# Kernel tuning notes

Measured on AMD Instinct MI355X. Metric: run time of the kernel, lower is better.

The kernel has to match this reference:

```python
import jax, jax.numpy as jnp
import numpy as np

B, N, M = 8, 2048, 2048
DQ = DK = DV = H = O = 1024

def setup_inputs() -> dict:
    key = jax.random.key(0)
    ks = jax.random.split(key, 10)
    input_query = jax.random.normal(ks[0], (B, N, DQ), dtype=jnp.float32)
    input_key = jax.random.normal(ks[1], (B, M, DK), dtype=jnp.float32)
    input_value = jax.random.normal(ks[2], (B, M, DV), dtype=jnp.float32)
    seq_lens = jax.random.randint(ks[3], (B,), 1, M + 1)
    seq_lens = seq_lens.at[0].set(M)  # original asserts max(seq_lens) == M
    s = 1.0 / np.sqrt(DQ)
    Wq = jax.random.normal(ks[4], (DQ, H), dtype=jnp.float32) * s
    bq = jnp.zeros((H,), dtype=jnp.float32)
    Wk = jax.random.normal(ks[5], (DK, H), dtype=jnp.float32) * s
    bk = jnp.zeros((H,), dtype=jnp.float32)
    Wv = jax.random.normal(ks[6], (DV, O), dtype=jnp.float32) * s
    bv = jnp.zeros((O,), dtype=jnp.float32)
    return {"input_query": input_query, "input_key": input_key, "input_value": input_value,
            "seq_lens": seq_lens, "Wq": Wq, "bq": bq, "Wk": Wk, "bk": bk, "Wv": Wv, "bv": bv}


def reference(input_query, input_key, input_value, seq_lens, Wq, bq, Wk, bk, Wv, bv):
    hidden_dim = Wq.shape[1]
    lq = input_query @ Wq + bq          # (B, N, H)
    lk = input_key @ Wk + bk            # (B, M, H)
    lv = input_value @ Wv + bv          # (B, M, O)
    scores = jnp.einsum('bnh,bmh->bnm', lq, lk) / jnp.sqrt(jnp.float32(hidden_dim))
    # additive mask: 0 for valid positions, finfo.min for padded (as in original)
    valid = (jnp.arange(scores.shape[-1]) < seq_lens[:, None])[:, None, :]  # (B,1,M)
    add_mask = jnp.where(valid, 0.0, jnp.finfo(scores.dtype).min)
    scores = scores + add_mask
    probs = jax.nn.softmax(scores, axis=-1)
    out = jnp.einsum('bnm,bmo->bno', probs, lv)  # dropout is identity in eval
    return out
```

## Files before the change

kernel.cpp:

```cpp
#include <hip/hip_runtime.h>
#include <hip/hip_bf16.h>

typedef unsigned short u16;
typedef __attribute__((ext_vector_type(8))) short bfrag;
typedef __attribute__((ext_vector_type(4))) float f32x4;
typedef __attribute__((ext_vector_type(8))) unsigned short us8;
typedef __attribute__((ext_vector_type(4))) unsigned short us4;

__device__ __forceinline__ u16 f2bf(float f) {
  union { float f; unsigned int u; } x; x.f = f;
  unsigned int r = x.u + 0x7fffu + ((x.u >> 16) & 1u);
  return (u16)(r >> 16);
}
__device__ __forceinline__ float bf2f(u16 u) {
  union { unsigned int u; float f; } x; x.u = ((unsigned int)u) << 16;
  return x.f;
}

__device__ __forceinline__ void gld16(const void* g, void* l) {
  __builtin_amdgcn_global_load_lds((const __attribute__((address_space(1))) void*)g,
                                   (__attribute__((address_space(3))) void*)l, 16, 0, 0);
}

__global__ __launch_bounds__(256) void transpose_w(const float* __restrict__ W0,
                                                   const float* __restrict__ W1,
                                                   const float* __restrict__ W2,
                                                   u16* __restrict__ T0,
                                                   u16* __restrict__ T1,
                                                   u16* __restrict__ T2) {
  const float* W = (blockIdx.z == 0) ? W0 : ((blockIdx.z == 1) ? W1 : W2);
  u16* T = (blockIdx.z == 0) ? T0 : ((blockIdx.z == 1) ? T1 : T2);
  __shared__ u16 tile[64][72];
  const int t = threadIdx.x;
  const int rr = t >> 4;
  const int cc = (t & 15) * 4;
  const int kbase = blockIdx.y * 64, nbase = blockIdx.x * 64;
#pragma unroll
  for (int j = 0; j < 4; ++j) {
    int kl = rr + j * 16;
    float4 v = *(const float4*)(W + (size_t)(kbase + kl) * 1024 + nbase + cc);
    tile[kl][cc + 0] = f2bf(v.x);
    tile[kl][cc + 1] = f2bf(v.y);
    tile[kl][cc + 2] = f2bf(v.z);
    tile[kl][cc + 3] = f2bf(v.w);
  }
  __syncthreads();
#pragma unroll
  for (int j = 0; j < 4; ++j) {
    int nl = rr + j * 16;
    us4 o;
    o[0] = tile[cc + 0][nl];
    o[1] = tile[cc + 1][nl];
    o[2] = tile[cc + 2][nl];
    o[3] = tile[cc + 3][nl];
    *(us4*)(T + (size_t)(nbase + nl) * 1024 + kbase + cc) = o;
  }
}

__global__ __launch_bounds__(256) void cvt_bf16(const float* __restrict__ src,
                                                u16* __restrict__ dst, int n8) {
  int i = blockIdx.x * blockDim.x + threadIdx.x;
  const int stride = gridDim.x * blockDim.x;
  for (; i < n8; i += stride) {
    const float4* p = (const float4*)(src + (size_t)i * 8);
    float4 v0 = p[0], v1 = p[1];
    us8 o;
    o[0] = f2bf(v0.x); o[1] = f2bf(v0.y); o[2] = f2bf(v0.z); o[3] = f2bf(v0.w);
    o[4] = f2bf(v1.x); o[5] = f2bf(v1.y); o[6] = f2bf(v1.z); o[7] = f2bf(v1.w);
    *(us8*)(dst + (size_t)i * 8) = o;
  }
}

template <int OUT>
__global__ __launch_bounds__(512, 2) void gemm256(const u16* __restrict__ gA,
                                                  const u16* __restrict__ gB,
                                                  const float* __restrict__ bias,
                                                  void* __restrict__ outp,
                                                  int K, int ldc) {
  __shared__ u16 lds[65536];
  const int tid = threadIdx.x;

  const int id = blockIdx.x + gridDim.x * blockIdx.y;
  const int bx = (id >> 3) & 3, by = (id & 7) + 8 * (id >> 5);

  const u16* A = gA;
  const u16* B = gB;
  const int brow = by * 256, bcol = bx * 256;

  const int wv = tid >> 6, l = tid & 63;
  const int wm = wv >> 2, wn = wv & 3;
  const int fr = l & 15, fq = l >> 4;
  const int g0 = (fq ^ (fr & 7)) * 8;
  const int g1 = ((4 + fq) ^ (fr & 7)) * 8;

  const int srow = tid >> 3;
  const int sg = (tid & 7) ^ (srow & 7);
  const u16* aS = A + (size_t)(brow + srow) * K + sg * 8;
  const u16* bS = B + (size_t)(bcol + srow) * K + sg * 8;
  u16* const dA = lds + wv * 512;
  u16* const dB = lds + 32768 + wv * 512;

  f32x4 acc[8][4] = {};
  const int NT = K >> 6;

  auto stA = [&](int tile, int c, int buf) {
    gld16(aS + (size_t)tile * 64 + (size_t)c * 64 * K, dA + buf * 16384 + c * 4096);
  };
  auto stB = [&](int tile, int c, int buf) {
    gld16(bS + (size_t)tile * 64 + (size_t)c * 64 * K, dB + buf * 16384 + c * 4096);
  };

#pragma unroll
  for (int c = 0; c < 4; ++c) stA(0, c, 0);
#pragma unroll
  for (int c = 0; c < 4; ++c) stB(0, c, 0);
  if (NT > 1) {
    stA(1, 0, 1); stA(1, 2, 1);
    stB(1, 0, 1); stB(1, 1, 1); stB(1, 2, 1); stB(1, 3, 1);
  }

  for (int t = 0; t < NT; ++t) {
    const int cur = t & 1;
    const u16* At = lds + cur * 16384;
    const u16* Bt = lds + 32768 + cur * 16384;

    if (t + 1 < NT) asm volatile("s_waitcnt vmcnt(6)" ::: "memory");
    else            asm volatile("s_waitcnt vmcnt(0)" ::: "memory");
    __builtin_amdgcn_s_barrier();

    bfrag a[4][2], b[2][2][2];

#pragma unroll
    for (int m = 0; m < 4; ++m) {
      const u16* p = At + (wm * 128 + m * 16 + fr) * 64;
      a[m][0] = *(const bfrag*)(p + g0);
      a[m][1] = *(const bfrag*)(p + g1);
    }
#pragma unroll
    for (int n = 0; n < 2; ++n) {
      const u16* p = Bt + (wn * 64 + n * 16 + fr) * 64;
      b[0][n][0] = *(const bfrag*)(p + g0);
      b[0][n][1] = *(const bfrag*)(p + g1);
    }
    if (t + 1 < NT) { stA(t + 1, 1, cur ^ 1); stA(t + 1, 3, cur ^ 1); }
    __builtin_amdgcn_s_barrier();
    asm volatile("s_waitcnt lgkmcnt(0)" ::: "memory");
    __builtin_amdgcn_sched_barrier(0);
    __builtin_amdgcn_s_setprio(1);
#pragma unroll
    for (int n = 0; n < 2; ++n)
#pragma unroll
      for (int m = 0; m < 4; ++m) {
        acc[m][n] = __builtin_amdgcn_mfma_f32_16x16x32_bf16(a[m][0], b[0][n][0], acc[m][n], 0, 0, 0);
        acc[m][n] = __builtin_amdgcn_mfma_f32_16x16x32_bf16(a[m][1], b[0][n][1], acc[m][n], 0, 0, 0);
      }
    __builtin_amdgcn_s_setprio(0);
    __builtin_amdgcn_s_barrier();

#pragma unroll
    for (int n = 0; n < 2; ++n) {
      const u16* p = Bt + (wn * 64 + 32 + n * 16 + fr) * 64;
      b[1][n][0] = *(const bfrag*)(p + g0);
      b[1][n][1] = *(const bfrag*)(p + g1);
    }
    if (t + 2 < NT) { stA(t + 2, 0, cur); stA(t + 2, 2, cur); }
    __builtin_amdgcn_s_barrier();
    asm volatile("s_waitcnt lgkmcnt(0)" ::: "memory");
    __builtin_amdgcn_sched_barrier(0);
    __builtin_amdgcn_s_setprio(1);
#pragma unroll
    for (int n = 0; n < 2; ++n)
#pragma unroll
      for (int m = 0; m < 4; ++m) {
        acc[m][2 + n] = __builtin_amdgcn_mfma_f32_16x16x32_bf16(a[m][0], b[1][n][0], acc[m][2 + n], 0, 0, 0);
        acc[m][2 + n] = __builtin_amdgcn_mfma_f32_16x16x32_bf16(a[m][1], b[1][n][1], acc[m][2 + n], 0, 0, 0);
      }
    __builtin_amdgcn_s_setprio(0);
    __builtin_amdgcn_s_barrier();

#pragma unroll
    for (int m = 0; m < 4; ++m) {
      const u16* p = At + (wm * 128 + 64 + m * 16 + fr) * 64;
      a[m][0] = *(const bfrag*)(p + g0);
      a[m][1] = *(const bfrag*)(p + g1);
    }
    if (t + 2 < NT) { stB(t + 2, 0, cur); stB(t + 2, 1, cur); }
    __builtin_amdgcn_s_barrier();
    asm volatile("s_waitcnt lgkmcnt(0)" ::: "memory");
    __builtin_amdgcn_sched_barrier(0);
    __builtin_amdgcn_s_setprio(1);
#pragma unroll
    for (int n = 0; n < 2; ++n)
#pragma unroll
      for (int m = 0; m < 4; ++m) {
        acc[4 + m][n] = __builtin_amdgcn_mfma_f32_16x16x32_bf16(a[m][0], b[0][n][0], acc[4 + m][n], 0, 0, 0);
        acc[4 + m][n] = __builtin_amdgcn_mfma_f32_16x16x32_bf16(a[m][1], b[0][n][1], acc[4 + m][n], 0, 0, 0);
      }
    __builtin_amdgcn_s_setprio(0);
    __builtin_amdgcn_s_barrier();

    if (t + 2 < NT) { stB(t + 2, 2, cur); stB(t + 2, 3, cur); }
    __builtin_amdgcn_s_setprio(1);
#pragma unroll
    for (int n = 0; n < 2; ++n)
#pragma unroll
      for (int m = 0; m < 4; ++m) {
        acc[4 + m][2 + n] = __builtin_amdgcn_mfma_f32_16x16x32_bf16(a[m][0], b[1][n][0], acc[4 + m][2 + n], 0, 0, 0);
        acc[4 + m][2 + n] = __builtin_amdgcn_mfma_f32_16x16x32_bf16(a[m][1], b[1][n][1], acc[4 + m][2 + n], 0, 0, 0);
      }
    __builtin_amdgcn_s_setprio(0);
    __builtin_amdgcn_s_barrier();
  }

#pragma unroll
  for (int mg = 0; mg < 8; ++mg) {
    const int r0 = brow + wm * 128 + mg * 16 + fq * 4;
#pragma unroll
    for (int n = 0; n < 4; ++n) {
      const int c = bcol + wn * 64 + n * 16 + fr;
      f32x4 vv = acc[mg][n];
      float bb = bias[c];
      if constexpr (OUT == 0) {
        u16* C = (u16*)outp;
#pragma unroll
        for (int j = 0; j < 4; ++j) C[(size_t)(r0 + j) * ldc + c] = f2bf(vv[j] + bb);
      } else {
        const int bz2 = r0 >> 11, mm = r0 & 2047;
        us4 o;
#pragma unroll
        for (int j = 0; j < 4; ++j) o[j] = f2bf(vv[j] + bb);
        *(us4*)((u16*)outp + ((size_t)bz2 * 1024 + c) * 2048 + mm) = o;
      }
    }
  }
}

template <int OUT>
__global__ __launch_bounds__(512, 4) void gemm128d(const u16* __restrict__ gA,
                                                   const u16* __restrict__ gB,
                                                   void* __restrict__ outp,
                                                   int K, int ldc,
                                                   size_t aStride, size_t bStride,
                                                   size_t cStride,
                                                   const int* __restrict__ seq) {
  __shared__ u16 lds[32768];
  const int tid = threadIdx.x;
  const int bx = blockIdx.x, by = blockIdx.y, bz = blockIdx.z;

  const u16* A = gA + (size_t)bz * aStride;
  const u16* B = gB + (size_t)bz * bStride;
  const int brow = by * 128, bcol = bx * 128;

  int NTe = K >> 6;
  if constexpr (OUT == 1) {
    if (bcol >= seq[bz]) return;
  }
  if constexpr (OUT == 3) {
    const int nt2 = (seq[bz] + 63) >> 6;
    NTe = nt2 < NTe ? nt2 : NTe;
  }

  const int wv = tid >> 6, l = tid & 63;
  const int wm = wv >> 2, wn = wv & 3;
  const int fr = l & 15, fq = l >> 4;
  const int g0 = (fq ^ (fr & 7)) * 8;
  const int g1 = ((4 + fq) ^ (fr & 7)) * 8;

  const int srow = tid >> 3;
  const int sg = (tid & 7) ^ (srow & 7);
  const u16* aS = A + (size_t)(brow + srow) * K + sg * 8;
  const u16* bS = B + (size_t)(bcol + srow) * K + sg * 8;
  u16* const dA = lds + wv * 512;
  u16* const dB = lds + 16384 + wv * 512;

  f32x4 acc[4][2] = {};

  auto stage = [&](int tile, int buf) {
#pragma unroll
    for (int c = 0; c < 2; ++c)
      gld16(aS + (size_t)tile * 64 + (size_t)c * 64 * K, dA + buf * 8192 + c * 4096);
#pragma unroll
    for (int c = 0; c < 2; ++c)
      gld16(bS + (size_t)tile * 64 + (size_t)c * 64 * K, dB + buf * 8192 + c * 4096);
  };

  stage(0, 0);
  asm volatile("s_waitcnt vmcnt(0)" ::: "memory");
  __builtin_amdgcn_s_barrier();

  for (int t = 0; t < NTe; ++t) {
    const int cur = t & 1;
    const u16* At = lds + cur * 8192;
    const u16* Bt = lds + 16384 + cur * 8192;

    if (t + 1 < NTe) stage(t + 1, cur ^ 1);

    bfrag a[4][2], b[2][2];
#pragma unroll
    for (int m = 0; m < 4; ++m) {
      const u16* p = At + (wm * 64 + m * 16 + fr) * 64;
      a[m][0] = *(const bfrag*)(p + g0);
      a[m][1] = *(const bfrag*)(p + g1);
    }
#pragma unroll
    for (int n = 0; n < 2; ++n) {
      const u16* p = Bt + (wn * 32 + n * 16 + fr) * 64;
      b[n][0] = *(const bfrag*)(p + g0);
      b[n][1] = *(const bfrag*)(p + g1);
    }
    asm volatile("s_waitcnt lgkmcnt(0)" ::: "memory");
    __builtin_amdgcn_sched_barrier(0);
    __builtin_amdgcn_s_setprio(1);
#pragma unroll
    for (int m = 0; m < 4; ++m)
#pragma unroll
      for (int n = 0; n < 2; ++n) {
        acc[m][n] = __builtin_amdgcn_mfma_f32_16x16x32_bf16(a[m][0], b[n][0], acc[m][n], 0, 0, 0);
        acc[m][n] = __builtin_amdgcn_mfma_f32_16x16x32_bf16(a[m][1], b[n][1], acc[m][n], 0, 0, 0);
      }
    __builtin_amdgcn_s_setprio(0);
    if (t + 1 < NTe) asm volatile("s_waitcnt vmcnt(0)" ::: "memory");
    __builtin_amdgcn_s_barrier();
  }

#pragma unroll
  for (int m = 0; m < 4; ++m) {
    const int r0 = brow + wm * 64 + m * 16 + fq * 4;
#pragma unroll
    for (int n = 0; n < 2; ++n) {
      const int c = bcol + wn * 32 + n * 16 + fr;
      f32x4 vv = acc[m][n];
      if constexpr (OUT == 1) {
        u16* C = (u16*)outp + (size_t)bz * cStride;
#pragma unroll
        for (int j = 0; j < 4; ++j) C[(size_t)(r0 + j) * ldc + c] = f2bf(vv[j] * 0.03125f);
      } else {
        float* C = (float*)outp + (size_t)bz * cStride;
#pragma unroll
        for (int j = 0; j < 4; ++j) C[(size_t)(r0 + j) * ldc + c] = vv[j];
      }
    }
  }
}

__global__ __launch_bounds__(256) void softmax_mask(u16* __restrict__ probs,
                                                    const int* __restrict__ seq) {
  const int bid = blockIdx.x;
  const int b = bid >> 11, n = bid & 2047;
  const int len = seq[b];
  const int len64 = (len + 63) & ~63;
  u16* row = probs + ((size_t)b * 2048 + n) * 2048;
  const int t = threadIdx.x;
  const int w = t >> 6, l = t & 63;

  us8 sv = {};
  if (t * 8 < len) sv = *(const us8*)(row + t * 8);
  float vals[8];
  float vmax = -1e30f;
#pragma unroll
  for (int e = 0; e < 8; ++e) {
    int m = t * 8 + e;
    float x = bf2f(sv[e]);
    vals[e] = (m < len) ? x : -1e30f;
    vmax = fmaxf(vmax, vals[e]);
  }
#pragma unroll
  for (int o = 32; o > 0; o >>= 1) vmax = fmaxf(vmax, __shfl_xor(vmax, o, 64));
  __shared__ float sm[4], ss[4];
  if (l == 0) sm[w] = vmax;
  __syncthreads();
  vmax = fmaxf(fmaxf(sm[0], sm[1]), fmaxf(sm[2], sm[3]));

  float ev[8];
  float sum = 0.f;
#pragma unroll
  for (int e = 0; e < 8; ++e) {
    int m = t * 8 + e;
    float p = (m < len) ? __expf(vals[e] - vmax) : 0.f;
    ev[e] = p;
    sum += p;
  }
#pragma unroll
  for (int o = 32; o > 0; o >>= 1) sum += __shfl_xor(sum, o, 64);
  if (l == 0) ss[w] = sum;
  __syncthreads();
  sum = ss[0] + ss[1] + ss[2] + ss[3];
  float inv = 1.f / sum;
  if (t * 8 < len64) {
    us8 ov;
#pragma unroll
    for (int e = 0; e < 8; ++e) ov[e] = f2bf(ev[e] * inv);
    *(us8*)(row + t * 8) = ov;
  }
}

extern "C" void kernel_launch(void* const* d_in, const int* in_sizes, int n_in,
                              void* d_out, int out_size, void* d_ws, size_t ws_size,
                              hipStream_t stream) {
  const float* q   = (const float*)d_in[0];
  const float* k   = (const float*)d_in[1];
  const float* v   = (const float*)d_in[2];
  const int*   seq = (const int*)d_in[3];
  const float* Wq  = (const float*)d_in[4];
  const float* bq  = (const float*)d_in[5];
  const float* Wk  = (const float*)d_in[6];
  const float* bk  = (const float*)d_in[7];
  const float* Wv  = (const float*)d_in[8];
  const float* bv  = (const float*)d_in[9];
  float* out = (float*)d_out;

  u16* ws = (u16*)d_ws;
  u16* wtq = ws;
  u16* wtk = wtq + (size_t)1024 * 1024;
  u16* wtv = wtk + (size_t)1024 * 1024;
  u16* lq  = wtv + (size_t)1024 * 1024;
  u16* lk  = lq + (size_t)16384 * 1024;
  u16* lvt = lk + (size_t)16384 * 1024;
  u16* probs = lvt + (size_t)16384 * 1024;
  u16* cbuf = probs;

  const size_t S21 = (size_t)2048 * 1024;
  const size_t S22 = (size_t)2048 * 2048;

  transpose_w<<<dim3(16, 16, 3), 256, 0, stream>>>(Wq, Wk, Wv, wtq, wtk, wtv);

  cvt_bf16<<<dim3(2048), 256, 0, stream>>>(q, cbuf, 2097152);
  gemm256<0><<<dim3(4, 64, 1), 512, 0, stream>>>(cbuf, wtq, bq, lq, 1024, 1024);
  cvt_bf16<<<dim3(2048), 256, 0, stream>>>(k, cbuf, 2097152);
  gemm256<0><<<dim3(4, 64, 1), 512, 0, stream>>>(cbuf, wtk, bk, lk, 1024, 1024);
  cvt_bf16<<<dim3(2048), 256, 0, stream>>>(v, cbuf, 2097152);
  gemm256<2><<<dim3(4, 64, 1), 512, 0, stream>>>(cbuf, wtv, bv, lvt, 1024, 1024);

  gemm128d<1><<<dim3(16, 16, 8), 512, 0, stream>>>(lq, lk, probs, 1024, 2048, S21, S21, S22, seq);
  softmax_mask<<<dim3(16384), 256, 0, stream>>>(probs, seq);
  gemm128d<3><<<dim3(8, 16, 8), 512, 0, stream>>>(probs, lvt, out, 2048, 1024, S22, S21, S21, seq);
}
```

Measured before the change: 328.4 us.

## Split-K the probs×V GEMM into two halves with a reduction pass

Result: slower. 351.7 us (+7.1%).

```diff
diff --git a/kernel.cpp b/kernel.cpp
--- a/kernel.cpp
+++ b/kernel.cpp
@@ -242,22 +242,30 @@
                                                    int K, int ldc,
                                                    size_t aStride, size_t bStride,
                                                    size_t cStride,
-                                                   const int* __restrict__ seq) {
+                                                   const int* __restrict__ seq,
+                                                   float* __restrict__ p1) {
   __shared__ u16 lds[32768];
   const int tid = threadIdx.x;
-  const int bx = blockIdx.x, by = blockIdx.y, bz = blockIdx.z;
+  const int bx = blockIdx.x, by = blockIdx.y;
+
+  int bz, half = 0;
+  if constexpr (OUT == 3) { bz = blockIdx.z & 7; half = blockIdx.z >> 3; }
+  else bz = blockIdx.z;
 
   const u16* A = gA + (size_t)bz * aStride;
   const u16* B = gB + (size_t)bz * bStride;
   const int brow = by * 128, bcol = bx * 128;
 
-  int NTe = K >> 6;
+  const int NT = K >> 6;
+  int t0 = 0, t1 = NT;
   if constexpr (OUT == 1) {
     if (bcol >= seq[bz]) return;
   }
   if constexpr (OUT == 3) {
-    const int nt2 = (seq[bz] + 63) >> 6;
-    NTe = nt2 < NTe ? nt2 : NTe;
+    int nt2 = (seq[bz] + 63) >> 6;
+    nt2 = nt2 < NT ? nt2 : NT;
+    if (half == 0) { t0 = 0; t1 = nt2 < 16 ? nt2 : 16; }
+    else           { if (nt2 <= 16) return; t0 = 16; t1 = nt2; }
   }
 
   const int wv = tid >> 6, l = tid & 63;
@@ -284,16 +292,16 @@
       gld16(bS + (size_t)tile * 64 + (size_t)c * 64 * K, dB + buf * 8192 + c * 4096);
   };
 
-  stage(0, 0);
+  stage(t0, t0 & 1);
   asm volatile("s_waitcnt vmcnt(0)" ::: "memory");
   __builtin_amdgcn_s_barrier();
 
-  for (int t = 0; t < NTe; ++t) {
+  for (int t = t0; t < t1; ++t) {
     const int cur = t & 1;
     const u16* At = lds + cur * 8192;
     const u16* Bt = lds + 16384 + cur * 8192;
 
-    if (t + 1 < NTe) stage(t + 1, cur ^ 1);
+    if (t + 1 < t1) stage(t + 1, cur ^ 1);
 
     bfrag a[4][2], b[2][2];
 #pragma unroll
@@ -319,7 +327,7 @@
         acc[m][n] = __builtin_amdgcn_mfma_f32_16x16x32_bf16(a[m][1], b[n][1], acc[m][n], 0, 0, 0);
       }
     __builtin_amdgcn_s_setprio(0);
-    if (t + 1 < NTe) asm volatile("s_waitcnt vmcnt(0)" ::: "memory");
+    if (t + 1 < t1) asm volatile("s_waitcnt vmcnt(0)" ::: "memory");
     __builtin_amdgcn_s_barrier();
   }
 
@@ -335,12 +343,24 @@
 #pragma unroll
         for (int j = 0; j < 4; ++j) C[(size_t)(r0 + j) * ldc + c] = f2bf(vv[j] * 0.03125f);
       } else {
-        float* C = (float*)outp + (size_t)bz * cStride;
+        float* C = (half ? p1 : (float*)outp) + (size_t)bz * cStride;
 #pragma unroll
         for (int j = 0; j < 4; ++j) C[(size_t)(r0 + j) * ldc + c] = vv[j];
       }
     }
   }
+}
+
+__global__ __launch_bounds__(256) void reduce_add(float* __restrict__ out,
+                                                  const float* __restrict__ p1,
+                                                  const int* __restrict__ seq) {
+  const int b = blockIdx.z;
+  if (seq[b] <= 1024) return;
+  const size_t base = (size_t)b * 2048 * 1024 + ((size_t)blockIdx.x * 256 + threadIdx.x) * 4;
+  float4 a = *(const float4*)(out + base);
+  float4 c = *(const float4*)(p1 + base);
+  a.x += c.x; a.y += c.y; a.z += c.z; a.w += c.w;
+  *(float4*)(out + base) = a;
 }
 
 __global__ __launch_bounds__(256) void softmax_mask(u16* __restrict__ probs,
@@ -418,6 +438,7 @@
   u16* lvt = lk + (size_t)16384 * 1024;
   u16* probs = lvt + (size_t)16384 * 1024;
   u16* cbuf = probs;
+  float* p1 = (float*)lq;
 
   const size_t S21 = (size_t)2048 * 1024;
   const size_t S22 = (size_t)2048 * 2048;
@@ -431,7 +452,10 @@
   cvt_bf16<<<dim3(2048), 256, 0, stream>>>(v, cbuf, 2097152);
   gemm256<2><<<dim3(4, 64, 1), 512, 0, stream>>>(cbuf, wtv, bv, lvt, 1024, 1024);
 
-  gemm128d<1><<<dim3(16, 16, 8), 512, 0, stream>>>(lq, lk, probs, 1024, 2048, S21, S21, S22, seq);
+  gemm128d<1><<<dim3(16, 16, 8), 512, 0, stream>>>(lq, lk, probs, 1024, 2048,
+                                                   S21, S21, S22, seq, nullptr);
   softmax_mask<<<dim3(16384), 256, 0, stream>>>(probs, seq);
-  gemm128d<3><<<dim3(8, 16, 8), 512, 0, stream>>>(probs, lvt, out, 2048, 1024, S22, S21, S21, seq);
-}
+  gemm128d<3><<<dim3(8, 16, 16), 512, 0, stream>>>(probs, lvt, out, 2048, 1024,
+                                                   S22, S21, S21, seq, p1);
+  reduce_add<<<dim3(2048, 1, 8), 256, 0, stream>>>(out, p1, seq);
+}
```
